# Kernel optimization log

Hardware: AMD Instinct MI355X
Metric: run time of the kernel (lower is better)

## Reference

```python
import jax, jax.numpy as jnp
import numpy as np

S = 64          # image_size / sdf cube side / embed dim
P = 4           # frame & sdf patch size
NC = 4          # number_of_couples
HP = 8          # num_heads
E = 32          # embedding_middle_attention
FC = 4          # final_number_of_channels
G = S // P      # 16 patches per side
N_FR = G * G * NC      # 1024 frame tokens
N_SDF = G ** 3         # 4096 sdf tokens
N = N_FR + N_SDF       # 5120 total tokens
NB = N // S            # 80 blocks


def setup_inputs() -> dict:
    key = jax.random.key(0)
    ks = jax.random.split(key, 12)
    s = 0.05  # keep attention logits numerically sane
    return {
        "cond1": jax.random.normal(ks[0], (1, 1, S, S, S), jnp.float32),
        "cond2": jax.random.uniform(ks[1], (1, 1, 4 * NC, S, S), jnp.float32),
        "W_emb": jax.random.normal(ks[2], (S, P * P * 4), jnp.float32) * s,   # Linear weight (out,in)
        "b_emb": jnp.zeros((S,), jnp.float32),
        "W_conv3d": jax.random.normal(ks[3], (S, 1, P, P, P), jnp.float32) * s,
        "b_conv3d": jnp.zeros((S,), jnp.float32),
        "pos_emb": jax.random.normal(ks[4], (N, S), jnp.float32) * s,
        "WQ": jax.random.normal(ks[5], (HP, S, E), jnp.float32) * s,
        "WK": jax.random.normal(ks[6], (HP, S, E), jnp.float32) * s,
        "WV": jax.random.normal(ks[7], (HP, S, E), jnp.float32) * s,
        "W_out": jax.random.normal(ks[8], (HP * E, S), jnp.float32) * s,
        "ln_gamma": jnp.ones((N, S), jnp.float32),
        "ln_beta": jnp.zeros((N, S), jnp.float32),
        "W_conv2d": jax.random.normal(ks[9], (S * FC, NB), jnp.float32) * s,  # 1x1 conv (out,in)
        "b_conv2d": jnp.zeros((S * FC,), jnp.float32),
    }


def _frames_to_patches(frames, W_emb, b_emb):
    # frames: (B,1,C,H,W) with C=4*NC, H=W=S
    b = frames.shape[0]
    x = frames[:, 0]                       # (B,C,S,S)
    x = x.transpose(0, 2, 3, 1)            # (B,S,S,C)
    x = x.reshape(b, G, P, G, P, 4 * NC)
    x = x.transpose(0, 1, 3, 2, 4, 5)      # (B,G,G,P,P,C)
    x = x.reshape(b, G * G, P, P, 4 * NC)
    x = x.transpose(0, 1, 4, 2, 3)         # (B,Np,C,P,P)
    # tensor_split along channels into NC chunks, cat along token dim
    x = x.reshape(b, G * G, NC, 4, P, P).transpose(0, 2, 1, 3, 4, 5)
    x = x.reshape(b, N_FR, 4 * P * P)      # flatten (c,i,j) row-major, matches torch
    return x @ W_emb.T + b_emb             # (B, N_FR, S)


def _sdf_to_patches(sdf, W_conv3d, b_conv3d):
    # Conv3d with kernel==stride==P is exact non-overlapping patching + matmul
    b = sdf.shape[0]
    x = sdf[:, 0]                                       # (B,S,S,S)
    x = x.reshape(b, G, P, G, P, G, P)
    x = x.transpose(0, 1, 3, 5, 2, 4, 6)                # (B,G,G,G,P,P,P)
    x = x.reshape(b, N_SDF, P ** 3)
    wc = W_conv3d.reshape(S, P ** 3)                    # (out, d*h*w), same flatten order
    return x @ wc.T + b_conv3d                          # (B, N_SDF, S)


def reference(cond1, cond2, W_emb, b_emb, W_conv3d, b_conv3d, pos_emb,
              WQ, WK, WV, W_out, ln_gamma, ln_beta, W_conv2d, b_conv2d):
    b = cond1.shape[0]
    fr = _frames_to_patches(cond2, W_emb, b_emb)        # (B,1024,64)
    sd = _sdf_to_patches(cond1, W_conv3d, b_conv3d)     # (B,4096,64)
    X = jnp.concatenate([sd, fr], axis=1) + pos_emb     # (B,N,64)

    # manual multi-head attention
    Q = jnp.einsum('bnd,hde->bhne', X, WQ)
    K = jnp.einsum('bnd,hde->bhne', X, WK)
    V = jnp.einsum('bnd,hde->bhne', X, WV)
    scores = jnp.einsum('bhne,bhme->bhnm', Q, K) / jnp.sqrt(jnp.float32(E))
    A = jax.nn.softmax(scores, axis=-1)
    O = jnp.einsum('bhnm,bhme->bhne', A, V)             # (B,H,N,E)
    O = O.transpose(0, 2, 1, 3).reshape(b, N, HP * E)   # head-order concat
    Xn = O @ W_out + X                                  # residual

    # LayerNorm over BOTH (N, emb) axes (torch LayerNorm((N,S)))
    mu = jnp.mean(Xn, axis=(1, 2), keepdims=True)
    var = jnp.mean(jnp.square(Xn - mu), axis=(1, 2), keepdims=True)
    Xn = (Xn - mu) / jnp.sqrt(var + 1e-5) * ln_gamma + ln_beta

    # adapt: reshape to blocks, 1x1 conv2d, reshape to volume
    Xr = Xn.reshape(b, NB, S, S)
    Xc = jnp.einsum('bchw,oc->bohw', Xr, W_conv2d) + b_conv2d[None, :, None, None]
    return Xc.reshape(b, FC, S, S, S)
```

## Files before the change

### kernel.cpp

```cpp
#include <hip/hip_runtime.h>
#include <hip/hip_bf16.h>

typedef short bf16x8 __attribute__((ext_vector_type(8)));
typedef float f32x4 __attribute__((ext_vector_type(4)));
typedef unsigned short u16;
typedef unsigned int u32;

#define NTOK 5120
#define NSDF 4096

__device__ __forceinline__ float b2f(u16 x){
  u32 u = ((u32)x) << 16; float f; __builtin_memcpy(&f, &u, 4); return f;
}
__device__ __forceinline__ u16 f2b(float f){
  u32 u; __builtin_memcpy(&u, &f, 4);
  return (u16)((u + 0x7fffu + ((u >> 16) & 1u)) >> 16);
}
__device__ __forceinline__ u32 cvtpk(float lo, float hi){
  u32 r;
  asm("v_cvt_pk_bf16_f32 %0, %1, %2" : "=v"(r) : "v"(lo), "v"(hi));
  return r;
}
__device__ __forceinline__ f32x4 mfma16(bf16x8 a, bf16x8 b, f32x4 c){
  return __builtin_amdgcn_mfma_f32_16x16x32_bf16(a, b, c, 0, 0, 0);
}
__device__ __forceinline__ void gld16(const void* g, void* l){
  __builtin_amdgcn_global_load_lds(
      (const __attribute__((address_space(1))) u32*)g,
      (__attribute__((address_space(3))) u32*)l, 16, 0, 0);
}

__global__ __launch_bounds__(256) void k_build_x(
    const float* __restrict__ cond1, const float* __restrict__ cond2,
    const float* __restrict__ W_emb, const float* __restrict__ b_emb,
    const float* __restrict__ W_c3, const float* __restrict__ b_c3,
    const float* __restrict__ pos, u16* __restrict__ Xout,
    const float* __restrict__ WQ, const float* __restrict__ WK,
    const float* __restrict__ WV, const float* __restrict__ W_out,
    const float* __restrict__ Wc,
    u16* __restrict__ Wt, u16* __restrict__ Wto, u16* __restrict__ Wcb)
{
  __shared__ __align__(16) u16 Psh[64][72];
  __shared__ __align__(16) u16 Wsh[64][72];
  int b = blockIdx.x, t = threadIdx.x;
  if (b >= 80){
    int gid = (b - 80) * 256 + t;
    const int gsz = 32 * 256;
    for (int i = gid; i < 49152; i += gsz){
      int m = i >> 14, r = i & 16383;
      int h = r >> 11, d = (r >> 5) & 63, e = r & 31;
      const float* src = (m == 0) ? WQ : ((m == 1) ? WK : WV);
      float v = src[(h * 64 + d) * 32 + e];
      if (m == 0) v *= 0.17677669529663689f * 1.4426950408889634f;
      Wt[((m * 8 + h) * 32 + e) * 64 + d] = f2b(v);
    }
    for (int i = gid; i < 16384; i += gsz){
      int k = i >> 6, d = i & 63;
      Wto[d * 256 + k] = f2b(W_out[i]);
    }
    for (int i = gid; i < 20480; i += gsz) Wcb[i] = f2b(Wc[i]);
    return;
  }
  bool sdb = (b < 64);
  {
    int nl = t >> 2, sub = t & 3;
    const float* src = sdb ? cond1 : cond2;
    int nn = sdb ? (b * 64 + nl) : (b * 64 + nl - NSDF);
    int g0 = nn >> 8, g1 = (nn >> 4) & 15, g2 = nn & 15;
    const float* sp = src + (g0 * 4 + sub) * 4096 + g1 * 4 * 64 + g2 * 4;
    for (int p1 = 0; p1 < 4; ++p1){
      float4 v = *(const float4*)(sp + p1 * 64);
      ushort4 o;
      o.x = f2b(v.x); o.y = f2b(v.y); o.z = f2b(v.z); o.w = f2b(v.w);
      *(ushort4*)&Psh[nl][sub * 16 + p1 * 4] = o;
    }
  }
  {
    const float* Wf = sdb ? W_c3 : W_emb;
    for (int i = t; i < 4096; i += 256)
      Wsh[i >> 6][i & 63] = f2b(Wf[i]);
  }
  __syncthreads();
  int w = t >> 6, lane = t & 63, l15 = lane & 15, g = lane >> 4;
  const float* bias = sdb ? b_c3 : b_emb;
  bf16x8 a0 = *(const bf16x8*)&Psh[w * 16 + l15][g * 8];
  bf16x8 a1 = *(const bf16x8*)&Psh[w * 16 + l15][32 + g * 8];
  for (int nb = 0; nb < 4; ++nb){
    bf16x8 b0 = *(const bf16x8*)&Wsh[nb * 16 + l15][g * 8];
    bf16x8 b1 = *(const bf16x8*)&Wsh[nb * 16 + l15][32 + g * 8];
    f32x4 acc = {0.f, 0.f, 0.f, 0.f};
    acc = mfma16(a0, b0, acc);
    acc = mfma16(a1, b1, acc);
    int d = nb * 16 + l15;
    float bs = bias[d];
    for (int r = 0; r < 4; ++r){
      int tok = b * 64 + w * 16 + g * 4 + r;
      float v = acc[r] + bs + pos[tok * 64 + d];
      Xout[tok * 64 + d] = f2b(v);
    }
  }
}

__global__ __launch_bounds__(256) void k_qkv(
    const u16* __restrict__ X, const u16* __restrict__ Wt,
    u16* __restrict__ Q, u16* __restrict__ K, u16* __restrict__ VT)
{
  __shared__ __align__(16) u16 Xsh[64][72];
  __shared__ __align__(16) u16 Vsh[4][32][72];
  int bid = blockIdx.x, b = bid / 6, grp = bid % 6;
  int t = threadIdx.x;
  {
    int nl = t >> 2, cb = t & 3;
    const u16* sp = X + (b * 64 + nl) * 64 + cb * 16;
    *(bf16x8*)&Xsh[nl][cb * 16] = *(const bf16x8*)(sp);
    *(bf16x8*)&Xsh[nl][cb * 16 + 8] = *(const bf16x8*)(sp + 8);
  }
  __syncthreads();
  int w = t >> 6, lane = t & 63, l15 = lane & 15, g = lane >> 4;
  int pair = grp * 4 + w, m = pair >> 3, h = pair & 7;
  bf16x8 a0[4], a1[4];
  for (int ms = 0; ms < 4; ++ms){
    a0[ms] = *(const bf16x8*)&Xsh[ms * 16 + l15][g * 8];
    a1[ms] = *(const bf16x8*)&Xsh[ms * 16 + l15][32 + g * 8];
  }
  if (grp < 4){
    for (int nb = 0; nb < 2; ++nb){
      const u16* wp = Wt + ((m * 8 + h) * 32 + nb * 16 + l15) * 64;
      bf16x8 b0 = *(const bf16x8*)(wp + g * 8);
      bf16x8 b1 = *(const bf16x8*)(wp + 32 + g * 8);
      int e = nb * 16 + l15;
      for (int ms = 0; ms < 4; ++ms){
        f32x4 acc = {0.f, 0.f, 0.f, 0.f};
        acc = mfma16(a0[ms], b0, acc);
        acc = mfma16(a1[ms], b1, acc);
        for (int r = 0; r < 4; ++r){
          int n = b * 64 + ms * 16 + g * 4 + r;
          u16 v = f2b(acc[r]);
          if (m == 0) Q[(h * NTOK + n) * 32 + e] = v;
          else        K[(h * NTOK + n) * 32 + e] = v;
        }
      }
    }
  } else {
    for (int nb = 0; nb < 2; ++nb){
      const u16* wp = Wt + ((2 * 8 + h) * 32 + nb * 16 + l15) * 64;
      bf16x8 b0 = *(const bf16x8*)(wp + g * 8);
      bf16x8 b1 = *(const bf16x8*)(wp + 32 + g * 8);
      int e = nb * 16 + l15;
      for (int ms = 0; ms < 4; ++ms){
        f32x4 acc = {0.f, 0.f, 0.f, 0.f};
        acc = mfma16(a0[ms], b0, acc);
        acc = mfma16(a1[ms], b1, acc);
        for (int r = 0; r < 4; ++r)
          Vsh[w][e][ms * 16 + g * 4 + r] = f2b(acc[r]);
      }
    }
    __syncthreads();
    int hl = t >> 6, e = (t >> 1) & 31, part = t & 1;
    int hglob = (grp - 4) * 4 + hl;
    const u16* src = &Vsh[hl][e][part * 32];
    u16* dst = VT + (size_t)(hglob * 32 + e) * NTOK + b * 64 + part * 32;
    #pragma unroll
    for (int j = 0; j < 4; ++j)
      *(uint4*)(dst + j * 8) = *(const uint4*)(src + j * 8);
  }
}

__global__ __launch_bounds__(256) void k_attn(
    const u16* __restrict__ Q, const u16* __restrict__ K, const u16* __restrict__ VT,
    u16* __restrict__ Opb, float* __restrict__ lpart)
{
  __shared__ __align__(16) u16 Ksh[2][128 * 32];
  __shared__ __align__(16) u16 Vsh[2][32 * 128];
  int bid = blockIdx.x;
  int x = bid & 7;
  int inner = bid >> 3;
  int qb = inner % 40;
  int p = x + 8 * (inner / 40);
  int sp = p >> 3, h = p & 7;
  int t = threadIdx.x, w = t >> 6, lane = t & 63, l15 = lane & 15, g = lane >> 4;
  int q0w = qb * 128 + w * 32;
  int kb = sp * 1280;
  int wb = w * 512;

  int rho0 = t >> 2, cpK = t & 3;
  int key0 = (rho0 & 0x60) | ((rho0 & 0x0C) << 1) | ((rho0 & 0x10) >> 2) | (rho0 & 3);
  int clogK = cpK ^ (rho0 & 3);
  const uint4* kg0 = (const uint4*)(K + (size_t)(h * NTOK + kb + key0) * 32 + clogK * 8);
  const uint4* kg1 = (const uint4*)(K + (size_t)(h * NTOK + kb + key0 + 64) * 32 + clogK * 8);
  int eV = t >> 4, cpV = t & 15;
  int clogV = cpV ^ eV;
  const uint4* vg0 = (const uint4*)(VT + (size_t)(h * 32 + eV) * NTOK + kb + clogV * 8);
  const uint4* vg1 = (const uint4*)(VT + (size_t)(h * 32 + eV + 16) * NTOK + kb + clogV * 8);

  bf16x8 qf0 = *(const bf16x8*)(Q + (size_t)(h * NTOK + q0w + l15) * 32 + g * 8);
  bf16x8 qf1 = *(const bf16x8*)(Q + (size_t)(h * NTOK + q0w + 16 + l15) * 32 + g * 8);

  union { u16 s[8]; bf16x8 v; } one8;
  #pragma unroll
  for (int j = 0; j < 8; ++j) one8.s[j] = 0x3F80;
  bf16x8 ones = one8.v;

  f32x4 oc[2][2];
  for (int u = 0; u < 2; ++u) for (int eb = 0; eb < 2; ++eb) oc[u][eb] = (f32x4){0.f,0.f,0.f,0.f};
  f32x4 als0 = {0.f,0.f,0.f,0.f}, als1 = {0.f,0.f,0.f,0.f};

  int kf_base = l15 * 32 + ((g ^ (l15 & 3)) * 8);

  gld16(kg0, &Ksh[0][wb]);
  gld16(kg1, &Ksh[0][wb + 2048]);
  gld16(vg0, &Vsh[0][wb]);
  gld16(vg1, &Vsh[0][wb + 2048]);

  for (int kt = 0; kt < 10; ++kt){
    int cur = kt & 1, nxt = cur ^ 1;
    if (kt < 9){
      gld16(kg0 + (kt + 1) * 512, &Ksh[nxt][wb]);
      gld16(kg1 + (kt + 1) * 512, &Ksh[nxt][wb + 2048]);
      gld16(vg0 + (kt + 1) * 16,  &Vsh[nxt][wb]);
      gld16(vg1 + (kt + 1) * 16,  &Vsh[nxt][wb + 2048]);
      asm volatile("s_waitcnt vmcnt(4)" ::: "memory");
    } else {
      asm volatile("s_waitcnt vmcnt(0)" ::: "memory");
    }
    __builtin_amdgcn_sched_barrier(0);
    __builtin_amdgcn_s_barrier();
    __builtin_amdgcn_sched_barrier(0);
    const u16* kB = &Ksh[cur][0];
    const u16* vB = &Vsh[cur][0];
    #pragma unroll
    for (int ks = 0; ks < 4; ++ks){
      f32x4 z = {0.f,0.f,0.f,0.f};
      bf16x8 kf0 = *(const bf16x8*)(kB + kf_base + ks * 1024);
      bf16x8 kf1 = *(const bf16x8*)(kB + kf_base + ks * 1024 + 512);
      f32x4 s0a = mfma16(kf0, qf0, z);
      f32x4 s1a = mfma16(kf1, qf0, z);
      f32x4 s0b = mfma16(kf0, qf1, z);
      f32x4 s1b = mfma16(kf1, qf1, z);
      int vf_off = l15 * 128 + (((ks * 4 + g) ^ l15) * 8);
      bf16x8 vf0 = *(const bf16x8*)(vB + vf_off);
      bf16x8 vf1 = *(const bf16x8*)(vB + vf_off + 2048);
      float pa0 = __builtin_amdgcn_exp2f(s0a[0]);
      float pa1 = __builtin_amdgcn_exp2f(s0a[1]);
      float pa2 = __builtin_amdgcn_exp2f(s0a[2]);
      float pa3 = __builtin_amdgcn_exp2f(s0a[3]);
      float pa4 = __builtin_amdgcn_exp2f(s1a[0]);
      float pa5 = __builtin_amdgcn_exp2f(s1a[1]);
      float pa6 = __builtin_amdgcn_exp2f(s1a[2]);
      float pa7 = __builtin_amdgcn_exp2f(s1a[3]);
      union { bf16x8 v; u32 wd[4]; } pua;
      pua.wd[0] = cvtpk(pa0, pa1); pua.wd[1] = cvtpk(pa2, pa3);
      pua.wd[2] = cvtpk(pa4, pa5); pua.wd[3] = cvtpk(pa6, pa7);
      float pb0 = __builtin_amdgcn_exp2f(s0b[0]);
      float pb1 = __builtin_amdgcn_exp2f(s0b[1]);
      float pb2 = __builtin_amdgcn_exp2f(s0b[2]);
      float pb3 = __builtin_amdgcn_exp2f(s0b[3]);
      float pb4 = __builtin_amdgcn_exp2f(s1b[0]);
      float pb5 = __builtin_amdgcn_exp2f(s1b[1]);
      float pb6 = __builtin_amdgcn_exp2f(s1b[2]);
      float pb7 = __builtin_amdgcn_exp2f(s1b[3]);
      union { bf16x8 v; u32 wd[4]; } pub;
      pub.wd[0] = cvtpk(pb0, pb1); pub.wd[1] = cvtpk(pb2, pb3);
      pub.wd[2] = cvtpk(pb4, pb5); pub.wd[3] = cvtpk(pb6, pb7);
      oc[0][0] = mfma16(pua.v, vf0, oc[0][0]);
      oc[0][1] = mfma16(pua.v, vf1, oc[0][1]);
      oc[1][0] = mfma16(pub.v, vf0, oc[1][0]);
      oc[1][1] = mfma16(pub.v, vf1, oc[1][1]);
      als0 = mfma16(pua.v, ones, als0);
      als1 = mfma16(pub.v, ones, als1);
    }
    __builtin_amdgcn_sched_barrier(0);
    __builtin_amdgcn_s_barrier();
  }

  u16* opp = Opb + ((size_t)(sp * 8 + h) * NTOK + q0w) * 32;
  for (int u = 0; u < 2; ++u)
    for (int eb = 0; eb < 2; ++eb)
      for (int r = 0; r < 4; ++r)
        opp[(u * 16 + 4 * g + r) * 32 + eb * 16 + l15] = f2b(oc[u][eb][r]);
  if (l15 == 0){
    float* lp = lpart + (size_t)(sp * 8 + h) * NTOK + q0w;
    #pragma unroll
    for (int r = 0; r < 4; ++r){
      lp[4 * g + r]      = als0[r];
      lp[16 + 4 * g + r] = als1[r];
    }
  }
}

__global__ __launch_bounds__(64) void k_xn(
    const u16* __restrict__ Opb, const float* __restrict__ lpart,
    const u16* __restrict__ Wto, const u16* __restrict__ X,
    float* __restrict__ Xn, float* __restrict__ partials)
{
  int b = blockIdx.x, lane = threadIdx.x, l15 = lane & 15, g = lane >> 4;
  int n0 = b * 16;
  int n = n0 + l15;
  f32x4 acc[4];
  #pragma unroll
  for (int nb = 0; nb < 4; ++nb) acc[nb] = (f32x4){0.f,0.f,0.f,0.f};
  #pragma unroll
  for (int ks = 0; ks < 8; ++ks){
    float l = lpart[(size_t)(0 * 8 + ks) * NTOK + n]
            + lpart[(size_t)(1 * 8 + ks) * NTOK + n]
            + lpart[(size_t)(2 * 8 + ks) * NTOK + n]
            + lpart[(size_t)(3 * 8 + ks) * NTOK + n];
    float rl = 1.0f / l;
    float ac0 = 0.f, ac1 = 0.f, ac2 = 0.f, ac3 = 0.f;
    float ac4 = 0.f, ac5 = 0.f, ac6 = 0.f, ac7 = 0.f;
    #pragma unroll
    for (int sp = 0; sp < 4; ++sp){
      union { bf16x8 v; u16 s[8]; } u;
      u.v = *(const bf16x8*)(Opb + (((size_t)(sp * 8 + ks) * NTOK + n) << 5) + g * 8);
      ac0 += b2f(u.s[0]); ac1 += b2f(u.s[1]); ac2 += b2f(u.s[2]); ac3 += b2f(u.s[3]);
      ac4 += b2f(u.s[4]); ac5 += b2f(u.s[5]); ac6 += b2f(u.s[6]); ac7 += b2f(u.s[7]);
    }
    union { bf16x8 v; u32 wd[4]; } m;
    m.wd[0] = cvtpk(ac0 * rl, ac1 * rl);
    m.wd[1] = cvtpk(ac2 * rl, ac3 * rl);
    m.wd[2] = cvtpk(ac4 * rl, ac5 * rl);
    m.wd[3] = cvtpk(ac6 * rl, ac7 * rl);
    bf16x8 av = m.v;
    #pragma unroll
    for (int nb = 0; nb < 4; ++nb){
      bf16x8 bb = *(const bf16x8*)(Wto + (nb * 16 + l15) * 256 + ks * 32 + g * 8);
      acc[nb] = mfma16(av, bb, acc[nb]);
    }
  }
  float s1 = 0.f, s2 = 0.f;
  #pragma unroll
  for (int nb = 0; nb < 4; ++nb){
    int d = nb * 16 + l15;
    #pragma unroll
    for (int r = 0; r < 4; ++r){
      int nn = n0 + g * 4 + r;
      float v = acc[nb][r] + b2f(X[nn * 64 + d]);
      Xn[nn * 64 + d] = v;
      s1 += v; s2 += v * v;
    }
  }
  for (int off = 1; off < 64; off <<= 1){
    s1 += __shfl_xor(s1, off);
    s2 += __shfl_xor(s2, off);
  }
  if (lane == 0){
    partials[b * 2]     = s1;
    partials[b * 2 + 1] = s2;
  }
}

__global__ __launch_bounds__(256) void k_out(
    const float* __restrict__ Xn, const float* __restrict__ partials,
    const float* __restrict__ gamma, const float* __restrict__ beta,
    const u16* __restrict__ Wcb, const float* __restrict__ bc,
    float* __restrict__ out)
{
  __shared__ float redA[8];
  __shared__ float murs2[2];
  __shared__ __align__(16) float Xs[80 * 16];
  int bid = blockIdx.x, t = threadIdx.x, w = t >> 6, lane = t & 63;
  int hh = bid >> 2, wq = (bid & 3) * 16;
  float s1 = 0.f, s2 = 0.f;
  for (int i = t; i < 320; i += 256){
    s1 += partials[2 * i];
    s2 += partials[2 * i + 1];
  }
  for (int off = 1; off < 64; off <<= 1){ s1 += __shfl_xor(s1, off); s2 += __shfl_xor(s2, off); }
  if (lane == 0){ redA[w * 2] = s1; redA[w * 2 + 1] = s2; }
  __syncthreads();
  if (t == 0){
    float S1 = redA[0] + redA[2] + redA[4] + redA[6];
    float S2 = redA[1] + redA[3] + redA[5] + redA[7];
    const float inv = 1.0f / 327680.0f;
    float mu = S1 * inv;
    murs2[0] = mu;
    murs2[1] = rsqrtf(S2 * inv - mu * mu + 1e-5f);
  }
  __syncthreads();
  float mu = murs2[0], rs = murs2[1];
  for (int i = t; i < 1280; i += 256){
    int c = i >> 4, ww = wq + (i & 15);
    int idx = (c * 64 + hh) * 64 + ww;
    Xs[i] = (Xn[idx] - mu) * rs * gamma[idx] + beta[idx];
  }
  __syncthreads();
  int o = t;
  const u16* wr = Wcb + o * 80;
  f32x4 acc4[4];
  for (int k = 0; k < 4; ++k) acc4[k] = (f32x4){0.f,0.f,0.f,0.f};
  for (int c = 0; c < 80; ++c){
    float wt = b2f(wr[c]);
    for (int k = 0; k < 4; ++k)
      acc4[k] += (*(const f32x4*)&Xs[c * 16 + k * 4]) * wt;
  }
  float bb = bc[o];
  for (int k = 0; k < 4; ++k)
    for (int j = 0; j < 4; ++j)
      out[o * 4096 + hh * 64 + wq + k * 4 + j] = acc4[k][j] + bb;
}

extern "C" void kernel_launch(void* const* d_in, const int* in_sizes, int n_in,
                              void* d_out, int out_size, void* d_ws, size_t ws_size,
                              hipStream_t stream) {
  const float* cond1 = (const float*)d_in[0];
  const float* cond2 = (const float*)d_in[1];
  const float* W_emb = (const float*)d_in[2];
  const float* b_emb = (const float*)d_in[3];
  const float* W_c3  = (const float*)d_in[4];
  const float* b_c3  = (const float*)d_in[5];
  const float* pos   = (const float*)d_in[6];
  const float* WQ    = (const float*)d_in[7];
  const float* WK    = (const float*)d_in[8];
  const float* WV    = (const float*)d_in[9];
  const float* W_out = (const float*)d_in[10];
  const float* gamma = (const float*)d_in[11];
  const float* beta  = (const float*)d_in[12];
  const float* Wc    = (const float*)d_in[13];
  const float* bc    = (const float*)d_in[14];
  float* out = (float*)d_out;
  char* ws = (char*)d_ws;

  u16*   X   = (u16*)(ws);
  u16*   Q   = (u16*)(ws +   655360);
  u16*   Kq  = (u16*)(ws +  3276800);
  u16*   VT  = (u16*)(ws +  5898240);
  float* Xn  = (float*)(ws + 11141120);
  u16*   Wt  = (u16*)(ws + 12451840);
  u16*   Wto = (u16*)(ws + 12550144);
  float* partials = (float*)(ws + 12582912);
  u16*   Wcb    = (u16*)(ws + 12601856);
  u16*   Opb    = (u16*)(ws + 12648448);
  float* lpart  = (float*)(ws + 23134208);

  k_build_x<<<112, 256, 0, stream>>>(cond1, cond2, W_emb, b_emb, W_c3, b_c3, pos, X,
                                     WQ, WK, WV, W_out, Wc, Wt, Wto, Wcb);
  k_qkv<<<480, 256, 0, stream>>>(X, Wt, Q, Kq, VT);
  k_attn<<<1280, 256, 0, stream>>>(Q, Kq, VT, Opb, lpart);
  k_xn<<<320, 64, 0, stream>>>(Opb, lpart, Wto, X, Xn, partials);
  k_out<<<256, 256, 0, stream>>>(Xn, partials, gamma, beta, Wcb, bc, out);
}
```

Before: 73.76 us.

## Fuse patch embedding into QKV kernel and move weight conversion into attention launch

Merges the patch-embedding kernel into the QKV projection kernel. Each block recomputes its 64-token X tile from the raw inputs, converts its own QKV weight fragments straight from fp32 global memory into registers, and only group 0 writes X out. The W_out and conv weight conversion moves to 8 extra blocks appended to the attention grid. This removes one kernel launch and the round trip of X and Wt through global memory. In exchange, the embedding matmul and pos loads are repeated six times per token block, and the weight reads are strided and uncoalesced.

```diff
diff --git a/kernel.cpp b/kernel.cpp
--- a/kernel.cpp
+++ b/kernel.cpp
@@ -30,38 +30,22 @@
       (__attribute__((address_space(3))) u32*)l, 16, 0, 0);
 }
 
-__global__ __launch_bounds__(256) void k_build_x(
+__global__ __launch_bounds__(256) void k_qkv(
     const float* __restrict__ cond1, const float* __restrict__ cond2,
     const float* __restrict__ W_emb, const float* __restrict__ b_emb,
     const float* __restrict__ W_c3, const float* __restrict__ b_c3,
-    const float* __restrict__ pos, u16* __restrict__ Xout,
+    const float* __restrict__ pos,
     const float* __restrict__ WQ, const float* __restrict__ WK,
-    const float* __restrict__ WV, const float* __restrict__ W_out,
-    const float* __restrict__ Wc,
-    u16* __restrict__ Wt, u16* __restrict__ Wto, u16* __restrict__ Wcb)
+    const float* __restrict__ WV,
+    u16* __restrict__ Xout, u16* __restrict__ Q, u16* __restrict__ K,
+    u16* __restrict__ VT)
 {
   __shared__ __align__(16) u16 Psh[64][72];
-  __shared__ __align__(16) u16 Wsh[64][72];
-  int b = blockIdx.x, t = threadIdx.x;
-  if (b >= 80){
-    int gid = (b - 80) * 256 + t;
-    const int gsz = 32 * 256;
-    for (int i = gid; i < 49152; i += gsz){
-      int m = i >> 14, r = i & 16383;
-      int h = r >> 11, d = (r >> 5) & 63, e = r & 31;
-      const float* src = (m == 0) ? WQ : ((m == 1) ? WK : WV);
-      float v = src[(h * 64 + d) * 32 + e];
-      if (m == 0) v *= 0.17677669529663689f * 1.4426950408889634f;
-      Wt[((m * 8 + h) * 32 + e) * 64 + d] = f2b(v);
-    }
-    for (int i = gid; i < 16384; i += gsz){
-      int k = i >> 6, d = i & 63;
-      Wto[d * 256 + k] = f2b(W_out[i]);
-    }
-    for (int i = gid; i < 20480; i += gsz) Wcb[i] = f2b(Wc[i]);
-    return;
-  }
+  __shared__ __align__(16) u16 Vsh[4][32][72];
+  int bid = blockIdx.x, b = bid / 6, grp = bid % 6;
+  int t = threadIdx.x, w = t >> 6, lane = t & 63, l15 = lane & 15, g = lane >> 4;
   bool sdb = (b < 64);
+
   {
     int nl = t >> 2, sub = t & 3;
     const float* src = sdb ? cond1 : cond2;
@@ -75,64 +59,74 @@
       *(ushort4*)&Psh[nl][sub * 16 + p1 * 4] = o;
     }
   }
-  {
-    const float* Wf = sdb ? W_c3 : W_emb;
-    for (int i = t; i < 4096; i += 256)
-      Wsh[i >> 6][i & 63] = f2b(Wf[i]);
-  }
-  __syncthreads();
-  int w = t >> 6, lane = t & 63, l15 = lane & 15, g = lane >> 4;
+  int pair = grp * 4 + w, m = pair >> 3, h = pair & 7;
+  const float* wsrc = ((m == 0) ? WQ : ((m == 1) ? WK : WV)) + h * 64 * 32;
+  float wscale = (m == 0) ? 0.17677669529663689f * 1.4426950408889634f : 1.0f;
+  bf16x8 wb0[2], wb1[2];
+  #pragma unroll
+  for (int nb = 0; nb < 2; ++nb){
+    union { bf16x8 v; u16 s[8]; } u0, u1;
+    #pragma unroll
+    for (int j = 0; j < 8; ++j){
+      u0.s[j] = f2b(wsrc[(g * 8 + j) * 32 + nb * 16 + l15] * wscale);
+      u1.s[j] = f2b(wsrc[(32 + g * 8 + j) * 32 + nb * 16 + l15] * wscale);
+    }
+    wb0[nb] = u0.v;
+    wb1[nb] = u1.v;
+  }
+  __syncthreads();
+
+  const float* Wf = sdb ? W_c3 : W_emb;
   const float* bias = sdb ? b_c3 : b_emb;
-  bf16x8 a0 = *(const bf16x8*)&Psh[w * 16 + l15][g * 8];
-  bf16x8 a1 = *(const bf16x8*)&Psh[w * 16 + l15][32 + g * 8];
+  bf16x8 pa0 = *(const bf16x8*)&Psh[w * 16 + l15][g * 8];
+  bf16x8 pa1 = *(const bf16x8*)&Psh[w * 16 + l15][32 + g * 8];
+  u16 xv[4][4];
+  #pragma unroll
   for (int nb = 0; nb < 4; ++nb){
-    bf16x8 b0 = *(const bf16x8*)&Wsh[nb * 16 + l15][g * 8];
-    bf16x8 b1 = *(const bf16x8*)&Wsh[nb * 16 + l15][32 + g * 8];
+    union { bf16x8 v; u16 s[8]; } e0, e1;
+    const float* wr = Wf + (nb * 16 + l15) * 64;
+    #pragma unroll
+    for (int j = 0; j < 8; ++j){
+      e0.s[j] = f2b(wr[g * 8 + j]);
+      e1.s[j] = f2b(wr[32 + g * 8 + j]);
+    }
     f32x4 acc = {0.f, 0.f, 0.f, 0.f};
-    acc = mfma16(a0, b0, acc);
-    acc = mfma16(a1, b1, acc);
+    acc = mfma16(pa0, e0.v, acc);
+    acc = mfma16(pa1, e1.v, acc);
     int d = nb * 16 + l15;
     float bs = bias[d];
+    #pragma unroll
     for (int r = 0; r < 4; ++r){
       int tok = b * 64 + w * 16 + g * 4 + r;
-      float v = acc[r] + bs + pos[tok * 64 + d];
-      Xout[tok * 64 + d] = f2b(v);
-    }
-  }
-}
-
-__global__ __launch_bounds__(256) void k_qkv(
-    const u16* __restrict__ X, const u16* __restrict__ Wt,
-    u16* __restrict__ Q, u16* __restrict__ K, u16* __restrict__ VT)
-{
-  __shared__ __align__(16) u16 Xsh[64][72];
-  __shared__ __align__(16) u16 Vsh[4][32][72];
-  int bid = blockIdx.x, b = bid / 6, grp = bid % 6;
-  int t = threadIdx.x;
-  {
-    int nl = t >> 2, cb = t & 3;
-    const u16* sp = X + (b * 64 + nl) * 64 + cb * 16;
-    *(bf16x8*)&Xsh[nl][cb * 16] = *(const bf16x8*)(sp);
-    *(bf16x8*)&Xsh[nl][cb * 16 + 8] = *(const bf16x8*)(sp + 8);
-  }
-  __syncthreads();
-  int w = t >> 6, lane = t & 63, l15 = lane & 15, g = lane >> 4;
-  int pair = grp * 4 + w, m = pair >> 3, h = pair & 7;
+      u16 xb = f2b(acc[r] + bs + pos[tok * 64 + d]);
+      xv[nb][r] = xb;
+      if (grp == 0) Xout[tok * 64 + d] = xb;
+    }
+  }
+  __syncthreads();
+  #pragma unroll
+  for (int nb = 0; nb < 4; ++nb)
+    #pragma unroll
+    for (int r = 0; r < 4; ++r)
+      Psh[w * 16 + g * 4 + r][nb * 16 + l15] = xv[nb][r];
+  __syncthreads();
+
   bf16x8 a0[4], a1[4];
+  #pragma unroll
   for (int ms = 0; ms < 4; ++ms){
-    a0[ms] = *(const bf16x8*)&Xsh[ms * 16 + l15][g * 8];
-    a1[ms] = *(const bf16x8*)&Xsh[ms * 16 + l15][32 + g * 8];
+    a0[ms] = *(const bf16x8*)&Psh[ms * 16 + l15][g * 8];
+    a1[ms] = *(const bf16x8*)&Psh[ms * 16 + l15][32 + g * 8];
   }
   if (grp < 4){
+    #pragma unroll
     for (int nb = 0; nb < 2; ++nb){
-      const u16* wp = Wt + ((m * 8 + h) * 32 + nb * 16 + l15) * 64;
-      bf16x8 b0 = *(const bf16x8*)(wp + g * 8);
-      bf16x8 b1 = *(const bf16x8*)(wp + 32 + g * 8);
       int e = nb * 16 + l15;
+      #pragma unroll
       for (int ms = 0; ms < 4; ++ms){
         f32x4 acc = {0.f, 0.f, 0.f, 0.f};
-        acc = mfma16(a0[ms], b0, acc);
-        acc = mfma16(a1[ms], b1, acc);
+        acc = mfma16(a0[ms], wb0[nb], acc);
+        acc = mfma16(a1[ms], wb1[nb], acc);
+        #pragma unroll
         for (int r = 0; r < 4; ++r){
           int n = b * 64 + ms * 16 + g * 4 + r;
           u16 v = f2b(acc[r]);
@@ -142,15 +136,15 @@
       }
     }
   } else {
+    #pragma unroll
     for (int nb = 0; nb < 2; ++nb){
-      const u16* wp = Wt + ((2 * 8 + h) * 32 + nb * 16 + l15) * 64;
-      bf16x8 b0 = *(const bf16x8*)(wp + g * 8);
-      bf16x8 b1 = *(const bf16x8*)(wp + 32 + g * 8);
       int e = nb * 16 + l15;
+      #pragma unroll
       for (int ms = 0; ms < 4; ++ms){
         f32x4 acc = {0.f, 0.f, 0.f, 0.f};
-        acc = mfma16(a0[ms], b0, acc);
-        acc = mfma16(a1[ms], b1, acc);
+        acc = mfma16(a0[ms], wb0[nb], acc);
+        acc = mfma16(a1[ms], wb1[nb], acc);
+        #pragma unroll
         for (int r = 0; r < 4; ++r)
           Vsh[w][e][ms * 16 + g * 4 + r] = f2b(acc[r]);
       }
@@ -168,17 +162,29 @@
 
 __global__ __launch_bounds__(256) void k_attn(
     const u16* __restrict__ Q, const u16* __restrict__ K, const u16* __restrict__ VT,
-    u16* __restrict__ Opb, float* __restrict__ lpart)
+    u16* __restrict__ Opb, float* __restrict__ lpart,
+    const float* __restrict__ W_out, const float* __restrict__ Wc,
+    u16* __restrict__ Wto, u16* __restrict__ Wcb)
 {
   __shared__ __align__(16) u16 Ksh[2][128 * 32];
   __shared__ __align__(16) u16 Vsh[2][32 * 128];
   int bid = blockIdx.x;
+  int t = threadIdx.x;
+  if (bid >= 1280){
+    int gid = (bid - 1280) * 256 + t;
+    for (int i = gid; i < 16384; i += 2048){
+      int k2 = i >> 6, d = i & 63;
+      Wto[d * 256 + k2] = f2b(W_out[i]);
+    }
+    for (int i = gid; i < 20480; i += 2048) Wcb[i] = f2b(Wc[i]);
+    return;
+  }
   int x = bid & 7;
   int inner = bid >> 3;
   int qb = inner % 40;
   int p = x + 8 * (inner / 40);
   int sp = p >> 3, h = p & 7;
-  int t = threadIdx.x, w = t >> 6, lane = t & 63, l15 = lane & 15, g = lane >> 4;
+  int w = t >> 6, lane = t & 63, l15 = lane & 15, g = lane >> 4;
   int q0w = qb * 128 + w * 32;
   int kb = sp * 1280;
   int wb = w * 512;
@@ -315,12 +321,12 @@
       ac0 += b2f(u.s[0]); ac1 += b2f(u.s[1]); ac2 += b2f(u.s[2]); ac3 += b2f(u.s[3]);
       ac4 += b2f(u.s[4]); ac5 += b2f(u.s[5]); ac6 += b2f(u.s[6]); ac7 += b2f(u.s[7]);
     }
-    union { bf16x8 v; u32 wd[4]; } m;
-    m.wd[0] = cvtpk(ac0 * rl, ac1 * rl);
-    m.wd[1] = cvtpk(ac2 * rl, ac3 * rl);
-    m.wd[2] = cvtpk(ac4 * rl, ac5 * rl);
-    m.wd[3] = cvtpk(ac6 * rl, ac7 * rl);
-    bf16x8 av = m.v;
+    union { bf16x8 v; u32 wd[4]; } mm;
+    mm.wd[0] = cvtpk(ac0 * rl, ac1 * rl);
+    mm.wd[1] = cvtpk(ac2 * rl, ac3 * rl);
+    mm.wd[2] = cvtpk(ac4 * rl, ac5 * rl);
+    mm.wd[3] = cvtpk(ac6 * rl, ac7 * rl);
+    bf16x8 av = mm.v;
     #pragma unroll
     for (int nb = 0; nb < 4; ++nb){
       bf16x8 bb = *(const bf16x8*)(Wto + (nb * 16 + l15) * 256 + ks * 32 + g * 8);
@@ -425,17 +431,15 @@
   u16*   Kq  = (u16*)(ws +  3276800);
   u16*   VT  = (u16*)(ws +  5898240);
   float* Xn  = (float*)(ws + 11141120);
-  u16*   Wt  = (u16*)(ws + 12451840);
   u16*   Wto = (u16*)(ws + 12550144);
   float* partials = (float*)(ws + 12582912);
   u16*   Wcb    = (u16*)(ws + 12601856);
   u16*   Opb    = (u16*)(ws + 12648448);
   float* lpart  = (float*)(ws + 23134208);
 
-  k_build_x<<<112, 256, 0, stream>>>(cond1, cond2, W_emb, b_emb, W_c3, b_c3, pos, X,
-                                     WQ, WK, WV, W_out, Wc, Wt, Wto, Wcb);
-  k_qkv<<<480, 256, 0, stream>>>(X, Wt, Q, Kq, VT);
-  k_attn<<<1280, 256, 0, stream>>>(Q, Kq, VT, Opb, lpart);
+  k_qkv<<<480, 256, 0, stream>>>(cond1, cond2, W_emb, b_emb, W_c3, b_c3, pos,
+                                 WQ, WK, WV, X, Q, Kq, VT);
+  k_attn<<<1288, 256, 0, stream>>>(Q, Kq, VT, Opb, lpart, W_out, Wc, Wto, Wcb);
   k_xn<<<320, 64, 0, stream>>>(Opb, lpart, Wto, X, Xn, partials);
   k_out<<<256, 256, 0, stream>>>(Xn, partials, gamma, beta, Wcb, bc, out);
 }
```

Result: no change. 73.19 us (median of 2 runs) (-0.8%).
